# Kernel tuning notes

Hardware: AMD Instinct MI355X
Metric: run time of the kernel (lower is better)

Reference implementation:

```python
import jax, jax.numpy as jnp
import numpy as np

U = 512  # units

def hard_sigmoid(x):
    # Keras hard_sigmoid: clip(0.2*x + 0.5, 0, 1)
    return jnp.clip(0.2 * x + 0.5, 0.0, 1.0)

def setup_inputs() -> dict:
    key = jax.random.key(0)
    ks = jax.random.split(key, 9)
    B, T, A, D = 64, 2048, 512, 512  # batch, annotation steps, annotation units, input dim
    s = lambda k, shape, scale: jax.random.normal(k, shape, jnp.float32) * scale
    return {
        "inputs": s(ks[0], (B, D), 1.0),
        "h": s(ks[1], (B, U), 1.0),
        "c": s(ks[2], (B, U), 1.0),
        "annotations": s(ks[3], (B, T, A), 1.0),
        "kernel": s(ks[4], (D + A, 4 * U), 0.02),
        "recurrent_kernel": s(ks[5], (U, 4 * U), 0.02),
        "bias": jnp.zeros((6 * U,), jnp.float32).at[U:2 * U].set(1.0),  # unit_forget_bias
        "kernel_u": s(ks[6], (A, U), 0.02),
        "kernel_w": s(ks[7], (U, U), 0.02),
        "kernel_v": s(ks[8], (U,), 0.02),
    }

def reference(inputs, h, c, annotations, kernel, recurrent_kernel, bias, kernel_u, kernel_w, kernel_v):
    bias_u = bias[4 * U:5 * U]
    # precomputed annotation projection (done once in build()): [B,T,U]
    uh = jnp.einsum('bta,au->btu', annotations, kernel_u) + bias_u
    # Bahdanau attention scores
    Wxstm = h @ kernel_w                                   # [B,U]
    et = jnp.einsum('btu,u->bt', jnp.tanh(uh + Wxstm[:, None, :]), kernel_v)
    at = jax.nn.softmax(et, axis=1)                        # exp/sum in source == softmax
    context = jnp.einsum('bt,bta->ba', at, annotations)    # [B,A]
    x = jnp.concatenate([inputs, context], axis=-1)        # [B, D+A]
    z = x @ kernel + h @ recurrent_kernel + bias[:4 * U]   # [B,4U]
    i = hard_sigmoid(z[:, :U])
    f = hard_sigmoid(z[:, U:2 * U])
    c_new = f * c + i * jnp.tanh(z[:, 2 * U:3 * U])
    o = hard_sigmoid(z[:, 3 * U:])
    h_new = o * jnp.tanh(c_new)
    return h_new
```

## Files before the change

### kernel.cpp

```cpp
#include <hip/hip_runtime.h>

constexpr int U = 512;
constexpr int B = 64;
constexpr int T = 2048;
constexpr int A = 512;

typedef __attribute__((ext_vector_type(8))) short short8;
typedef __attribute__((ext_vector_type(4))) float f32x4;

__device__ __forceinline__ unsigned short f32_to_bf16(float f) {
    unsigned int b = __float_as_uint(f);
    unsigned int r = (b + 0x7FFFu + ((b >> 16) & 1u)) >> 16;
    return (unsigned short)r;
}

__device__ __forceinline__ float fast_tanh(float x) {
    float e = exp2f(x * 2.885390081777927f);
    return (e - 1.0f) * __builtin_amdgcn_rcpf(e + 1.0f);
}

__device__ __forceinline__ float hard_sigmoid(float z) {
    return fminf(fmaxf(0.2f * z + 0.5f, 0.0f), 1.0f);
}

#define SB() __builtin_amdgcn_sched_barrier(0)

__global__ __launch_bounds__(256) void k_prep_s(const float* __restrict__ h,
                                                const float* __restrict__ kw,
                                                float* __restrict__ Sp) {
    int b = blockIdx.x >> 2;
    int kc = blockIdx.x & 3;
    int u = threadIdx.x;
    const float* hb = h + b * U + kc * 128;
    const float* kwb = kw + (size_t)kc * 128 * U;
    float a0 = 0.f, a1 = 0.f;
#pragma unroll 4
    for (int k = 0; k < 128; ++k) {
        float hv = hb[k];
        a0 += hv * kwb[(size_t)k * U + u];
        a1 += hv * kwb[(size_t)k * U + u + 256];
    }
    float* p = Sp + ((size_t)kc * 64 + b) * U;
    p[u] = a0;
    p[u + 256] = a1;
}

__global__ __launch_bounds__(256) void k_s_reduce(const float* __restrict__ Sp,
                                                  const float* __restrict__ bias,
                                                  float* __restrict__ S) {
    int gid = blockIdx.x * 256 + threadIdx.x;
    int b = gid >> 9, u = gid & 511;
    float s = bias[4 * U + u];
#pragma unroll
    for (int kc = 0; kc < 4; ++kc) s += Sp[((size_t)kc * 64 + b) * U + u];
    S[gid] = s;
}

__global__ __launch_bounds__(256) void k_prep_kpack(const float* __restrict__ ku,
                                                    unsigned short* __restrict__ kpack) {
    int t = blockIdx.x >> 3;
    int gid = (blockIdx.x & 7) * 256 + threadIdx.x;
    int d = gid >> 9;
    int u = gid & 511;
    float vals[8];
#pragma unroll
    for (int e = 0; e < 8; ++e) vals[e] = ku[(size_t)(t * 32 + d * 8 + e) * U + u];
    int sc = d ^ ((u >> 1) & 3);
    short8 pk;
#pragma unroll
    for (int e = 0; e < 8; ++e) pk[e] = (short)f32_to_bf16(vals[e]);
    *(short8*)&kpack[(size_t)t * 16384 + u * 32 + sc * 8] = pk;
}

__global__ __launch_bounds__(256) void k_prep_wt(const float* __restrict__ kern,
                                                 const float* __restrict__ rk,
                                                 unsigned short* __restrict__ Wt) {
    __shared__ float tile[32][33];
    int k0 = blockIdx.x << 5;
    int j0 = blockIdx.y << 5;
    int c = threadIdx.x & 31, r0 = threadIdx.x >> 5;
#pragma unroll
    for (int p = 0; p < 4; ++p) {
        int r = r0 + p * 8;
        int k = k0 + r;
        float val = (k < 1024) ? kern[k * 2048 + j0 + c]
                               : rk[(k - 1024) * 2048 + j0 + c];
        tile[r][c] = val;
    }
    __syncthreads();
#pragma unroll
    for (int p = 0; p < 4; ++p) {
        int r = r0 + p * 8;
        Wt[(size_t)(j0 + r) * 1536 + k0 + c] = f32_to_bf16(tile[c][r]);
    }
}

__global__ __launch_bounds__(512, 2) void k_gemm_et(const float* __restrict__ ann,
                                                    const unsigned short* __restrict__ kpack,
                                                    const float* __restrict__ S,
                                                    const float* __restrict__ v,
                                                    float* __restrict__ mz,
                                                    float* __restrict__ part) {
    __shared__ unsigned short As[2][128 * 32];
    __shared__ unsigned short Bs[3][512 * 32];
    __shared__ float red[8][64];
    __shared__ float elds[128];
    __shared__ float p_lds[128];

    const int tid = threadIdx.x;
    const int wave = tid >> 6;
    const int lane = tid & 63;
    const int lanelo = lane & 15;
    const int quad = lane >> 4;
    const int wr = wave >> 2;
    const int wc = wave & 3;

    const int mt = blockIdx.x;
    const int b = mt >> 4;
    const float* aBase = ann + (size_t)mt * 128 * A;
    const char* kpB = (const char*)kpack;

    f32x4 acc[4][8];
#pragma unroll
    for (int i = 0; i < 4; ++i)
#pragma unroll
        for (int j = 0; j < 8; ++j) acc[i][j] = {0.f, 0.f, 0.f, 0.f};

    const int rowA = tid >> 2;
    const int c8A = tid & 3;
    f32x4 pv0, pv1;

    auto load_a = [&](int kk) {
        const float* src = aBase + (size_t)rowA * A + kk + c8A * 8;
        pv0 = *(const f32x4*)src;
        pv1 = *(const f32x4*)(src + 4);
    };
    auto stage_b = [&](int t, int buf) {
        const char* src = kpB + (size_t)t * 32768;
#pragma unroll
        for (int p = 0; p < 4; ++p) {
            int seg = p * 8 + wave;
            __builtin_amdgcn_global_load_lds(
                (const __attribute__((address_space(1))) void*)(src + seg * 1024 + lane * 16),
                (__attribute__((address_space(3))) void*)((char*)&Bs[buf][0] + seg * 1024),
                16, 0, 0);
        }
    };
    auto cvt_store = [&](int buf) {
        short8 pk;
        pk[0] = (short)f32_to_bf16(pv0.x);
        pk[1] = (short)f32_to_bf16(pv0.y);
        pk[2] = (short)f32_to_bf16(pv0.z);
        pk[3] = (short)f32_to_bf16(pv0.w);
        pk[4] = (short)f32_to_bf16(pv1.x);
        pk[5] = (short)f32_to_bf16(pv1.y);
        pk[6] = (short)f32_to_bf16(pv1.z);
        pk[7] = (short)f32_to_bf16(pv1.w);
        *(short8*)&As[buf][rowA * 32 + ((c8A ^ ((rowA >> 1) & 3)) * 8)] = pk;
    };

    load_a(0);
    SB();
    stage_b(0, 0);
    SB();
    asm volatile("s_waitcnt vmcnt(4)" ::: "memory");
    SB();
    cvt_store(0);
    SB();
    stage_b(1, 1);
    SB();
    asm volatile("s_waitcnt vmcnt(4)" ::: "memory");
    asm volatile("s_waitcnt lgkmcnt(0)" ::: "memory");
    __builtin_amdgcn_s_barrier();

#pragma unroll
    for (int t = 0; t < 16; ++t) {
        const int cur = t & 1;
        const int curB = t % 3;

        SB();
        if (t < 15) load_a((t + 1) * 32);
        SB();
        if (t < 14) stage_b(t + 2, (t + 2) % 3);
        SB();

        short8 af[4];
#pragma unroll
        for (int mi = 0; mi < 4; ++mi) {
            int row = wr * 64 + mi * 16 + lanelo;
            af[mi] = *(const short8*)&As[cur][row * 32 + ((quad ^ ((row >> 1) & 3)) * 8)];
        }
        short8 bfr[8];
#pragma unroll
        for (int ni = 0; ni < 8; ++ni) {
            int rowb = wc * 128 + ni * 16 + lanelo;
            bfr[ni] = *(const short8*)&Bs[curB][rowb * 32 + ((quad ^ ((rowb >> 1) & 3)) * 8)];
        }
        asm volatile("s_waitcnt lgkmcnt(0)" ::: "memory");
        SB();

        __builtin_amdgcn_s_setprio(1);
#pragma unroll
        for (int mi = 0; mi < 4; ++mi)
#pragma unroll
            for (int ni = 0; ni < 8; ++ni)
                acc[mi][ni] = __builtin_amdgcn_mfma_f32_16x16x32_bf16(
                    af[mi], bfr[ni], acc[mi][ni], 0, 0, 0);
        __builtin_amdgcn_s_setprio(0);
        SB();

        if (t < 15) {
            if (t == 14) { asm volatile("s_waitcnt vmcnt(0)" ::: "memory"); }
            else         { asm volatile("s_waitcnt vmcnt(4)" ::: "memory"); }
            SB();
            cvt_store((t + 1) & 1);
        }
        asm volatile("s_waitcnt lgkmcnt(0)" ::: "memory");
        __builtin_amdgcn_s_barrier();
    }

    float rows[16];
#pragma unroll
    for (int i = 0; i < 16; ++i) rows[i] = 0.f;
#pragma unroll
    for (int ni = 0; ni < 8; ++ni) {
        int u = wc * 128 + ni * 16 + lanelo;
        float sv = S[b * U + u];
        float vv = v[u];
#pragma unroll
        for (int mi = 0; mi < 4; ++mi)
#pragma unroll
            for (int r = 0; r < 4; ++r)
                rows[mi * 4 + r] += fast_tanh(acc[mi][ni][r] + sv) * vv;
    }
#pragma unroll
    for (int i = 0; i < 16; ++i) {
        rows[i] += __shfl_xor(rows[i], 1);
        rows[i] += __shfl_xor(rows[i], 2);
        rows[i] += __shfl_xor(rows[i], 4);
        rows[i] += __shfl_xor(rows[i], 8);
    }
    if (lanelo == 0) {
#pragma unroll
        for (int mi = 0; mi < 4; ++mi)
#pragma unroll
            for (int r = 0; r < 4; ++r)
                red[wave][mi * 16 + quad * 4 + r] = rows[mi * 4 + r];
    }
    __syncthreads();

    if (tid < 128) {
        int wrr = tid >> 6;
        int m = tid & 63;
        elds[tid] = red[wrr * 4 + 0][m] + red[wrr * 4 + 1][m] +
                    red[wrr * 4 + 2][m] + red[wrr * 4 + 3][m];
    }
    __syncthreads();

    if (tid < 64) {
        float e0 = elds[tid];
        float e1 = elds[tid + 64];
        float m = fmaxf(e0, e1);
#pragma unroll
        for (int o = 1; o < 64; o <<= 1) m = fmaxf(m, __shfl_xor(m, o));
        float p0 = exp2f((e0 - m) * 1.4426950408889634f);
        float p1 = exp2f((e1 - m) * 1.4426950408889634f);
        float z = p0 + p1;
#pragma unroll
        for (int o = 1; o < 64; o <<= 1) z += __shfl_xor(z, o);
        p_lds[tid] = p0;
        p_lds[tid + 64] = p1;
        if (tid == 0) { mz[mt * 2] = m; mz[mt * 2 + 1] = z; }
    }
    __syncthreads();

    float* cbuf = (float*)&As[0][0];
    {
        int tg = tid >> 7;
        int a4 = (tid & 127) << 2;
        f32x4 cacc = {0.f, 0.f, 0.f, 0.f};
#pragma unroll 4
        for (int t2 = tg; t2 < 128; t2 += 4) {
            float w = p_lds[t2];
            f32x4 rv = *(const f32x4*)(aBase + (size_t)t2 * A + a4);
            cacc.x += w * rv.x;
            cacc.y += w * rv.y;
            cacc.z += w * rv.z;
            cacc.w += w * rv.w;
        }
        *(f32x4*)&cbuf[tg * 512 + a4] = cacc;
    }
    __syncthreads();
    {
        int a = tid;
        float s = cbuf[a] + cbuf[512 + a] + cbuf[1024 + a] + cbuf[1536 + a];
        part[(size_t)mt * 512 + a] = s;
    }
}

__global__ __launch_bounds__(256) void k_ctx_merge_xb(const float* __restrict__ part,
                                                      const float* __restrict__ mz,
                                                      const float* __restrict__ inputs,
                                                      const float* __restrict__ h,
                                                      unsigned short* __restrict__ xb) {
    int b = blockIdx.x;
    int tid = threadIdx.x;
    __shared__ float wsh[16];
    __shared__ float sinvZ;
    if (tid < 16) {
        float m_i = mz[(b * 16 + tid) * 2];
        float z_i = mz[(b * 16 + tid) * 2 + 1];
        float M = m_i;
#pragma unroll
        for (int o = 1; o < 16; o <<= 1) M = fmaxf(M, __shfl_xor(M, o));
        float w = exp2f((m_i - M) * 1.4426950408889634f);
        float wz = w * z_i;
#pragma unroll
        for (int o = 1; o < 16; o <<= 1) wz += __shfl_xor(wz, o);
        wsh[tid] = w;
        if (tid == 0) sinvZ = 1.0f / wz;
    }
    __syncthreads();
    float invZ = sinvZ;
    unsigned short* xrow = xb + (size_t)b * 1536;
#pragma unroll
    for (int i = 0; i < 2; ++i) {
        int a = tid + i * 256;
        float s = 0.f;
#pragma unroll
        for (int c2 = 0; c2 < 16; ++c2)
            s += wsh[c2] * part[((size_t)b * 16 + c2) * 512 + a];
        xrow[512 + a] = f32_to_bf16(s * invZ);
        xrow[a] = f32_to_bf16(inputs[b * 512 + a]);
        xrow[1024 + a] = f32_to_bf16(h[b * 512 + a]);
    }
}

__global__ __launch_bounds__(256) void k_zgemm(const unsigned short* __restrict__ xb,
                                               const unsigned short* __restrict__ Wt,
                                               float* __restrict__ zpart) {
    const int kc = blockIdx.x & 7;
    const int nt = blockIdx.x >> 3;
    const int wave = threadIdx.x >> 6;
    const int lane = threadIdx.x & 63;
    const int lanelo = lane & 15;
    const int quad = lane >> 4;

    const int n = nt * 64 + wave * 16 + lanelo;
    const unsigned short* bp = Wt + (size_t)n * 1536 + kc * 192 + quad * 8;
    const unsigned short* ap = xb + (size_t)lanelo * 1536 + kc * 192 + quad * 8;

    f32x4 acc[4];
#pragma unroll
    for (int i = 0; i < 4; ++i) acc[i] = {0.f, 0.f, 0.f, 0.f};

#pragma unroll
    for (int ks = 0; ks < 6; ++ks) {
        short8 bfrag = *(const short8*)(bp + ks * 32);
#pragma unroll
        for (int mi = 0; mi < 4; ++mi) {
            short8 afrag = *(const short8*)(ap + (size_t)mi * 16 * 1536 + ks * 32);
            acc[mi] = __builtin_amdgcn_mfma_f32_16x16x32_bf16(afrag, bfrag, acc[mi], 0, 0, 0);
        }
    }

    float* p = zpart + (size_t)kc * 64 * 2048;
#pragma unroll
    for (int mi = 0; mi < 4; ++mi)
#pragma unroll
        for (int r = 0; r < 4; ++r) {
            int m = mi * 16 + quad * 4 + r;
            p[(size_t)m * 2048 + n] = acc[mi][r];
        }
}

__global__ __launch_bounds__(256) void k_gates(const float* __restrict__ zpart,
                                               const float* __restrict__ bias,
                                               const float* __restrict__ c,
                                               float* __restrict__ hnew) {
    int gid = blockIdx.x * 256 + threadIdx.x;
    int b = gid >> 9;
    int u = gid & 511;
    float z[4];
#pragma unroll
    for (int g = 0; g < 4; ++g) {
        int j = (g << 9) + u;
        float s = bias[j];
#pragma unroll
        for (int kc = 0; kc < 8; ++kc)
            s += zpart[((size_t)kc * 64 + b) * 2048 + j];
        z[g] = s;
    }
    float ig = hard_sigmoid(z[0]);
    float fg = hard_sigmoid(z[1]);
    float cn = fg * c[b * 512 + u] + ig * fast_tanh(z[2]);
    float og = hard_sigmoid(z[3]);
    hnew[b * 512 + u] = og * fast_tanh(cn);
}

extern "C" void kernel_launch(void* const* d_in, const int* in_sizes, int n_in,
                              void* d_out, int out_size, void* d_ws, size_t ws_size,
                              hipStream_t stream) {
    const float* inputs = (const float*)d_in[0];
    const float* h      = (const float*)d_in[1];
    const float* c      = (const float*)d_in[2];
    const float* ann    = (const float*)d_in[3];
    const float* kern   = (const float*)d_in[4];
    const float* rk     = (const float*)d_in[5];
    const float* bias   = (const float*)d_in[6];
    const float* ku     = (const float*)d_in[7];
    const float* kw     = (const float*)d_in[8];
    const float* kv     = (const float*)d_in[9];

    char* ws = (char*)d_ws;
    float*          S     = (float*)(ws + 0);
    unsigned short* kpack = (unsigned short*)(ws + 131072);
    float*          mz    = (float*)(ws + 655360);
    float*          part  = (float*)(ws + 663552);
    float*          Sp    = (float*)(ws + 2760704);
    unsigned short* xb    = (unsigned short*)(ws + 3284992);
    unsigned short* Wt    = (unsigned short*)(ws + 3481600);
    float*          zpart = (float*)(ws + 9773056);
    float*          hnew  = (float*)d_out;

    k_prep_wt<<<dim3(48, 64), 256, 0, stream>>>(kern, rk, Wt);
    k_prep_kpack<<<128, 256, 0, stream>>>(ku, kpack);
    k_prep_s<<<256, 256, 0, stream>>>(h, kw, Sp);
    k_s_reduce<<<128, 256, 0, stream>>>(Sp, bias, S);
    k_gemm_et<<<1024, 512, 0, stream>>>(ann, kpack, S, kv, mz, part);
    k_ctx_merge_xb<<<64, 256, 0, stream>>>(part, mz, inputs, h, xb);
    k_zgemm<<<256, 256, 0, stream>>>(xb, Wt, zpart);
    k_gates<<<128, 256, 0, stream>>>(zpart, bias, c, hnew);
}
```

Measured before the change: 489.5 us.

## Split attention context reduction out of score GEMM into separate kernel

Moves the softmax-weighted context accumulation out of the fused score GEMM kernel: the GEMM now writes per-tile unnormalized probabilities to a workspace buffer, and a new kernel with twice as many blocks re-reads annotations to compute partial contexts. The merge kernel is updated to combine 32 partials per batch. This shortens the heavy GEMM kernel and spreads the context pass over more blocks, but annotations must be re-read from memory rather than while still cached after the GEMM, and an extra launch is added.

Result: slower. 504.7 us (+3.1%).

```diff
diff --git a/kernel.cpp b/kernel.cpp
--- a/kernel.cpp
+++ b/kernel.cpp
@@ -100,12 +100,11 @@
                                                     const float* __restrict__ S,
                                                     const float* __restrict__ v,
                                                     float* __restrict__ mz,
-                                                    float* __restrict__ part) {
+                                                    float* __restrict__ pvec) {
     __shared__ unsigned short As[2][128 * 32];
     __shared__ unsigned short Bs[3][512 * 32];
     __shared__ float red[8][64];
     __shared__ float elds[128];
-    __shared__ float p_lds[128];
 
     const int tid = threadIdx.x;
     const int wave = tid >> 6;
@@ -268,34 +267,40 @@
         float z = p0 + p1;
 #pragma unroll
         for (int o = 1; o < 64; o <<= 1) z += __shfl_xor(z, o);
-        p_lds[tid] = p0;
-        p_lds[tid + 64] = p1;
+        pvec[(size_t)mt * 128 + tid] = p0;
+        pvec[(size_t)mt * 128 + 64 + tid] = p1;
         if (tid == 0) { mz[mt * 2] = m; mz[mt * 2 + 1] = z; }
     }
+}
+
+__global__ __launch_bounds__(256) void k_ctx_part2(const float* __restrict__ pvec,
+                                                   const float* __restrict__ ann,
+                                                   float* __restrict__ part) {
+    __shared__ float buf[2][512];
+    int mt = blockIdx.x >> 1;
+    int tc = blockIdx.x & 1;
+    int half = threadIdx.x >> 7;
+    int a4 = (threadIdx.x & 127) << 2;
+    const float* annb = ann + ((size_t)mt * 128 + tc * 64) * A;
+    const float* pv = pvec + (size_t)mt * 128 + tc * 64;
+    f32x4 acc = {0.f, 0.f, 0.f, 0.f};
+#pragma unroll 8
+    for (int t = half; t < 64; t += 2) {
+        float w = pv[t];
+        f32x4 rv = *(const f32x4*)(annb + (size_t)t * A + a4);
+        acc.x += w * rv.x;
+        acc.y += w * rv.y;
+        acc.z += w * rv.z;
+        acc.w += w * rv.w;
+    }
+    *(f32x4*)&buf[half][a4] = acc;
     __syncthreads();
-
-    float* cbuf = (float*)&As[0][0];
-    {
-        int tg = tid >> 7;
-        int a4 = (tid & 127) << 2;
-        f32x4 cacc = {0.f, 0.f, 0.f, 0.f};
-#pragma unroll 4
-        for (int t2 = tg; t2 < 128; t2 += 4) {
-            float w = p_lds[t2];
-            f32x4 rv = *(const f32x4*)(aBase + (size_t)t2 * A + a4);
-            cacc.x += w * rv.x;
-            cacc.y += w * rv.y;
-            cacc.z += w * rv.z;
-            cacc.w += w * rv.w;
-        }
-        *(f32x4*)&cbuf[tg * 512 + a4] = cacc;
-    }
-    __syncthreads();
-    {
-        int a = tid;
-        float s = cbuf[a] + cbuf[512 + a] + cbuf[1024 + a] + cbuf[1536 + a];
-        part[(size_t)mt * 512 + a] = s;
-    }
+    int a2 = threadIdx.x << 1;
+    float s0 = buf[0][a2] + buf[1][a2];
+    float s1 = buf[0][a2 + 1] + buf[1][a2 + 1];
+    float* p = part + (size_t)blockIdx.x * 512;
+    p[a2] = s0;
+    p[a2 + 1] = s1;
 }
 
 __global__ __launch_bounds__(256) void k_ctx_merge_xb(const float* __restrict__ part,
@@ -328,8 +333,8 @@
         int a = tid + i * 256;
         float s = 0.f;
 #pragma unroll
-        for (int c2 = 0; c2 < 16; ++c2)
-            s += wsh[c2] * part[((size_t)b * 16 + c2) * 512 + a];
+        for (int c2 = 0; c2 < 32; ++c2)
+            s += wsh[c2 >> 1] * part[((size_t)b * 32 + c2) * 512 + a];
         xrow[512 + a] = f32_to_bf16(s * invZ);
         xrow[a] = f32_to_bf16(inputs[b * 512 + a]);
         xrow[1024 + a] = f32_to_bf16(h[b * 512 + a]);
@@ -416,18 +421,20 @@
     float*          S     = (float*)(ws + 0);
     unsigned short* kpack = (unsigned short*)(ws + 131072);
     float*          mz    = (float*)(ws + 655360);
-    float*          part  = (float*)(ws + 663552);
-    float*          Sp    = (float*)(ws + 2760704);
-    unsigned short* xb    = (unsigned short*)(ws + 3284992);
-    unsigned short* Wt    = (unsigned short*)(ws + 3481600);
-    float*          zpart = (float*)(ws + 9773056);
+    float*          pvec  = (float*)(ws + 663552);
+    float*          part  = (float*)(ws + 1187840);
+    float*          Sp    = (float*)(ws + 5382144);
+    unsigned short* xb    = (unsigned short*)(ws + 5906432);
+    unsigned short* Wt    = (unsigned short*)(ws + 6103040);
+    float*          zpart = (float*)(ws + 12394496);
     float*          hnew  = (float*)d_out;
 
     k_prep_wt<<<dim3(48, 64), 256, 0, stream>>>(kern, rk, Wt);
     k_prep_kpack<<<128, 256, 0, stream>>>(ku, kpack);
     k_prep_s<<<256, 256, 0, stream>>>(h, kw, Sp);
     k_s_reduce<<<128, 256, 0, stream>>>(Sp, bias, S);
-    k_gemm_et<<<1024, 512, 0, stream>>>(ann, kpack, S, kv, mz, part);
+    k_gemm_et<<<1024, 512, 0, stream>>>(ann, kpack, S, kv, mz, pvec);
+    k_ctx_part2<<<2048, 256, 0, stream>>>(pvec, ann, part);
     k_ctx_merge_xb<<<64, 256, 0, stream>>>(part, mz, inputs, h, xb);
     k_zgemm<<<256, 256, 0, stream>>>(xb, Wt, zpart);
     k_gates<<<128, 256, 0, stream>>>(zpart, bias, c, hnew);
```
